# Kernel tuning notes

Measured on AMD Instinct MI355X. Metric: run time of the kernel, lower is better.

Reference implementation:

```python
import jax, jax.numpy as jnp
import numpy as np

B, S, D = 4, 2048, 512
H, DK = 8, 64
EPS = 1e-8


def setup_inputs() -> dict:
    key = jax.random.key(0)
    ks = jax.random.split(key, 11)
    sc = 1.0 / np.sqrt(D)
    Q = jax.random.normal(ks[0], (B, S, D), dtype=jnp.float32)
    # binary keep-mask over key positions, [B, S]
    attention_masks = (jax.random.uniform(ks[1], (B, S)) > 0.1).astype(jnp.float32)
    Wq = jax.random.normal(ks[2], (D, H * DK), dtype=jnp.float32) * sc
    bq = jax.random.normal(ks[3], (H * DK,), dtype=jnp.float32) * 0.01
    Wk = jax.random.normal(ks[4], (D, H * DK), dtype=jnp.float32) * sc
    bk = jax.random.normal(ks[5], (H * DK,), dtype=jnp.float32) * 0.01
    Wv = jax.random.normal(ks[6], (D, H * DK), dtype=jnp.float32) * sc
    bv = jax.random.normal(ks[7], (H * DK,), dtype=jnp.float32) * 0.01
    Wo = jax.random.normal(ks[8], (H * DK, D), dtype=jnp.float32) * (1.0 / np.sqrt(H * DK))
    bo = jax.random.normal(ks[9], (D,), dtype=jnp.float32) * 0.01
    return {"Q": Q, "attention_masks": attention_masks, "Wq": Wq, "bq": bq,
            "Wk": Wk, "bk": bk, "Wv": Wv, "bv": bv, "Wo": Wo, "bo": bo}


def reference(Q, attention_masks, Wq, bq, Wk, bk, Wv, bv, Wo, bo):
    b, s, _ = Q.shape
    # projections -> [B, H, S, DK]
    q = (Q @ Wq + bq).reshape(b, s, H, DK).transpose(0, 2, 1, 3)
    k = (Q @ Wk + bk).reshape(b, s, H, DK).transpose(0, 2, 1, 3)
    v = (Q @ Wv + bv).reshape(b, s, H, DK).transpose(0, 2, 1, 3)
    # scores: exp(QK^T / sqrt(dk)) * mask, normalized by row-sum (no max subtraction, matching source)
    scores = jnp.exp(jnp.einsum('bhqd,bhkd->bhqk', q, k) / np.sqrt(DK))
    scores = scores * attention_masks[:, None, None, :]  # mask broadcast over query dim
    attn = scores / (jnp.sum(scores, axis=-1, keepdims=True) + EPS)
    ctx = jnp.einsum('bhqk,bhkd->bhqd', attn, v)
    ctx = ctx.transpose(0, 2, 1, 3).reshape(b, s, H * DK)
    return ctx @ Wo + bo
```

## Files before the change

### kernel.cpp

```cpp
#include <hip/hip_runtime.h>
#include <math.h>

constexpr int NB = 4, NS = 2048, ND = 512, NH = 8, NDK = 64;
constexpr int NM = NB * NS, NHD = NH * NDK;

typedef short short8v __attribute__((ext_vector_type(8)));
typedef float f32x16v __attribute__((ext_vector_type(16)));
typedef unsigned int uint4v __attribute__((ext_vector_type(4)));

__device__ __forceinline__ unsigned short f2bf(float f) {
    unsigned u = __float_as_uint(f);
    return (unsigned short)((u + 0x7fffu + ((u >> 16) & 1u)) >> 16);
}
__device__ __forceinline__ float bf2f(unsigned short h) {
    return __uint_as_float(((unsigned)h) << 16);
}

#define MFMA32(a, b, c) __builtin_amdgcn_mfma_f32_32x32x16_bf16(a, b, c, 0, 0, 0)

__global__ __launch_bounds__(256) void split_x(
    const float* __restrict__ X, unsigned short* __restrict__ xh,
    unsigned short* __restrict__ xl)
{
    const size_t base = ((size_t)blockIdx.x * 256 + threadIdx.x) * 16;
#pragma unroll
    for (int j = 0; j < 4; ++j) {
        float4 v = *(const float4*)&X[base + 4 * j];
        ushort4 h, l;
        h.x = f2bf(v.x); h.y = f2bf(v.y); h.z = f2bf(v.z); h.w = f2bf(v.w);
        l.x = f2bf(v.x - bf2f(h.x)); l.y = f2bf(v.y - bf2f(h.y));
        l.z = f2bf(v.z - bf2f(h.z)); l.w = f2bf(v.w - bf2f(h.w));
        *(ushort4*)&xh[base + 4 * j] = h;
        *(ushort4*)&xl[base + 4 * j] = l;
    }
}

__global__ __launch_bounds__(256) void split_wT(
    const float* __restrict__ W0, const float* __restrict__ W1,
    const float* __restrict__ W2, const float* __restrict__ W3,
    unsigned short* __restrict__ wth, unsigned short* __restrict__ wtl)
{
    const int z = blockIdx.z;
    const float* W = (z == 0) ? W0 : (z == 1) ? W1 : (z == 2) ? W2 : W3;
    unsigned short* th = wth + (size_t)z * ND * ND;
    unsigned short* tl = wtl + (size_t)z * ND * ND;

    __shared__ float T[64][68];
    const int t = threadIdx.x;
    const int k0 = blockIdx.y * 64, n0 = blockIdx.x * 64;
    {
        const int r = t >> 2, c4 = (t & 3) * 16;
#pragma unroll
        for (int j = 0; j < 4; ++j)
            *(float4*)&T[r][c4 + 4 * j] = *(const float4*)&W[(size_t)(k0 + r) * ND + n0 + c4 + 4 * j];
    }
    __syncthreads();
    {
        const int r = t >> 2, c4 = (t & 3) * 16;
        unsigned short* dh = th + (size_t)(n0 + r) * ND + k0 + c4;
        unsigned short* dl = tl + (size_t)(n0 + r) * ND + k0 + c4;
#pragma unroll
        for (int j = 0; j < 4; ++j) {
            ushort4 h, l;
#pragma unroll
            for (int e = 0; e < 4; ++e) {
                float v = T[c4 + 4 * j + e][r];
                unsigned short hh = f2bf(v);
                ((unsigned short*)&h)[e] = hh;
                ((unsigned short*)&l)[e] = f2bf(v - bf2f(hh));
            }
            *(ushort4*)(dh + 4 * j) = h;
            *(ushort4*)(dl + 4 * j) = l;
        }
    }
}

__global__ __launch_bounds__(256, 2) void proj_qkv_mfma(
    const unsigned short* __restrict__ xh, const unsigned short* __restrict__ xl,
    const unsigned short* __restrict__ wth, const unsigned short* __restrict__ wtl,
    const float* __restrict__ bq, const float* __restrict__ bk,
    const float* __restrict__ bv,
    unsigned short* __restrict__ qh, unsigned short* __restrict__ ql,
    unsigned short* __restrict__ kh, unsigned short* __restrict__ kl,
    unsigned short* __restrict__ vh)
{
    constexpr int AH = 0, AL = 16384, BH = 32768, BL = 49152;
    __shared__ __align__(16) unsigned char smem[65536];

    const int z = blockIdx.z;
    const float* bias = (z == 0) ? bq : (z == 1) ? bk : bv;
    unsigned short* hp = (z == 0) ? qh : (z == 1) ? kh : vh;
    unsigned short* lp = (z == 0) ? ql : (z == 1) ? kl : (unsigned short*)0;
    const float sc = (z == 0) ? 0.18033688011112042f : 1.0f;
    const unsigned char* bth = (const unsigned char*)(wth + (size_t)z * ND * ND);
    const unsigned char* btl = (const unsigned char*)(wtl + (size_t)z * ND * ND);

    const int tid = threadIdx.x, lane = tid & 63, w = tid >> 6;
    const int wm = w >> 1, wn = w & 1;
    const int c = lane & 31, hi = lane >> 5;
    const int m0 = blockIdx.y * 128, n0 = blockIdx.x * 128;

    const unsigned char* ah_base = (const unsigned char*)xh;
    const unsigned char* al_base = (const unsigned char*)xl;

    int rr[4], gg[4], dd[4];
#pragma unroll
    for (int i = 0; i < 4; ++i) {
        int G = tid + 256 * i;
        rr[i] = G >> 3; gg[i] = G & 7;
        dd[i] = rr[i] * 128 + ((gg[i] ^ (rr[i] & 7)) * 16);
    }

    uint4v sah[4], sal[4], sbh[4], sbl[4];
    auto loads = [&](int kt) {
        const int kb = kt * 128;
#pragma unroll
        for (int i = 0; i < 4; ++i) {
            const size_t arow = (size_t)(m0 + rr[i]) * 1024 + kb + gg[i] * 16;
            const size_t brow = (size_t)(n0 + rr[i]) * 1024 + kb + gg[i] * 16;
            sah[i] = *(const uint4v*)(ah_base + arow);
            sal[i] = *(const uint4v*)(al_base + arow);
            sbh[i] = *(const uint4v*)(bth + brow);
            sbl[i] = *(const uint4v*)(btl + brow);
        }
    };
    auto writes = [&]() {
#pragma unroll
        for (int i = 0; i < 4; ++i) {
            *(uint4v*)(smem + AH + dd[i]) = sah[i];
            *(uint4v*)(smem + AL + dd[i]) = sal[i];
            *(uint4v*)(smem + BH + dd[i]) = sbh[i];
            *(uint4v*)(smem + BL + dd[i]) = sbl[i];
        }
    };

    f32x16v acc[2][2];
#pragma unroll
    for (int a = 0; a < 2; ++a)
#pragma unroll
        for (int bq2 = 0; bq2 < 2; ++bq2)
#pragma unroll
            for (int r = 0; r < 16; ++r) acc[a][bq2][r] = 0.f;

    loads(0);
    for (int kt = 0; kt < ND / 64; ++kt) {
        __syncthreads();
        writes();
        if (kt + 1 < ND / 64) loads(kt + 1);
        __syncthreads();
#pragma unroll
        for (int ks = 0; ks < 4; ++ks) {
            short8v afh[2], afl[2], bfh[2], bfl[2];
#pragma unroll
            for (int ms = 0; ms < 2; ++ms) {
                const int row = wm * 64 + ms * 32 + c;
                const int gb = row * 128 + (((2 * ks + hi) ^ (c & 7)) * 16);
                afh[ms] = *(const short8v*)(smem + AH + gb);
                afl[ms] = *(const short8v*)(smem + AL + gb);
            }
#pragma unroll
            for (int ns = 0; ns < 2; ++ns) {
                const int row = wn * 64 + ns * 32 + c;
                const int gb = row * 128 + (((2 * ks + hi) ^ (c & 7)) * 16);
                bfh[ns] = *(const short8v*)(smem + BH + gb);
                bfl[ns] = *(const short8v*)(smem + BL + gb);
            }
#pragma unroll
            for (int ms = 0; ms < 2; ++ms)
#pragma unroll
                for (int ns = 0; ns < 2; ++ns) {
                    acc[ms][ns] = MFMA32(afh[ms], bfh[ns], acc[ms][ns]);
                    acc[ms][ns] = MFMA32(afh[ms], bfl[ns], acc[ms][ns]);
                    acc[ms][ns] = MFMA32(afl[ms], bfh[ns], acc[ms][ns]);
                }
        }
    }

    const int b = m0 >> 11;
    const int s_base = (m0 & (NS - 1)) + wm * 64;
#pragma unroll
    for (int ns = 0; ns < 2; ++ns) {
        const int n = n0 + wn * 64 + ns * 32 + c;
        const int h = n >> 6, dk = n & (NDK - 1);
        const float bv4 = bias[n];
        const size_t bhBase = (size_t)(b * NH + h) * NS * NDK + dk;
#pragma unroll
        for (int ms = 0; ms < 2; ++ms)
#pragma unroll
            for (int r = 0; r < 16; ++r) {
                const int s = s_base + ms * 32 + (r & 3) + 8 * (r >> 2) + 4 * hi;
                const float v = (acc[ms][ns][r] + bv4) * sc;
                const unsigned short h0 = f2bf(v);
                hp[bhBase + (size_t)s * NDK] = h0;
                if (lp) lp[bhBase + (size_t)s * NDK] = f2bf(v - bf2f(h0));
            }
    }
}

__global__ __launch_bounds__(256) void vt_convert(
    const unsigned short* __restrict__ vh, unsigned short* __restrict__ vth)
{
    const int bh = blockIdx.y;
    const int s0 = blockIdx.x * 64;
    __shared__ unsigned short th[64][72];
    const int t = threadIdx.x;
    {
        const int sl = t & 63, ch = (t >> 6) * 16;
        const unsigned short* sh = vh + ((size_t)bh * NS + s0 + sl) * NDK + ch;
#pragma unroll
        for (int j = 0; j < 4; ++j)
            *(ushort4*)&th[sl][ch + 4 * j] = *(const ushort4*)(sh + 4 * j);
    }
    __syncthreads();
    {
        const int dv = t >> 2, sc = (t & 3) * 16;
        unsigned short* dh = vth + ((size_t)bh * NDK + dv) * NS + s0 + sc;
#pragma unroll
        for (int j = 0; j < 4; ++j) {
            ushort4 oh;
            oh.x = th[sc + 4 * j + 0][dv]; oh.y = th[sc + 4 * j + 1][dv];
            oh.z = th[sc + 4 * j + 2][dv]; oh.w = th[sc + 4 * j + 3][dv];
            *(ushort4*)(dh + 4 * j) = oh;
        }
    }
}

__global__ __launch_bounds__(256, 2) void attn(
    const unsigned short* __restrict__ qhp, const unsigned short* __restrict__ qlp,
    const unsigned short* __restrict__ khp, const unsigned short* __restrict__ klp,
    const unsigned short* __restrict__ vthp,
    const float* __restrict__ maskp,
    unsigned short* __restrict__ cth)
{
    constexpr int NT = NS / 64;
    constexpr int KH = 0, KL = 8192, VH = 16384, TILE = 24576;
    constexpr int P_OFF = 49152;
    __shared__ __align__(16) unsigned char smem[59392];

    const int tid = threadIdx.x, lane = tid & 63, w = tid >> 6;
    const int bid = blockIdx.x;
    const int xcd = bid & 7, r0 = bid >> 3;
    const int qt = r0 & 15, bh = xcd + 8 * (r0 >> 4);
    const int b = bh >> 3;
    const int q0 = qt * 128;
    const int c = lane & 31, hi = lane >> 5;
    const int csw = (c & 7) * 16;

    unsigned* Ph = (unsigned*)(smem + P_OFF + w * 2560);

    const unsigned char* kh_base = (const unsigned char*)khp + (size_t)bh * NS * 128;
    const unsigned char* kl_base = (const unsigned char*)klp + (size_t)bh * NS * 128;
    const unsigned char* vh_base = (const unsigned char*)vthp + (size_t)bh * 64 * 4096;

    const int G1 = tid, G2 = tid + 256;
    const int r1 = G1 >> 3, g1 = G1 & 7, r2 = G2 >> 3, g2 = G2 & 7;
    const int d1 = r1 * 128 + ((g1 ^ (r1 & 7)) * 16);
    const int d2 = r2 * 128 + ((g2 ^ (r2 & 7)) * 16);

    uint4v skh1, skl1, svh1, skh2, skl2, svh2;
    auto loads = [&](int kt) {
        const size_t ko = (size_t)kt * 8192;
        const size_t vo = (size_t)kt * 128;
        skh1 = *(const uint4v*)(kh_base + ko + (size_t)G1 * 16);
        skh2 = *(const uint4v*)(kh_base + ko + (size_t)G2 * 16);
        skl1 = *(const uint4v*)(kl_base + ko + (size_t)G1 * 16);
        skl2 = *(const uint4v*)(kl_base + ko + (size_t)G2 * 16);
        svh1 = *(const uint4v*)(vh_base + vo + (size_t)r1 * 4096 + g1 * 16);
        svh2 = *(const uint4v*)(vh_base + vo + (size_t)r2 * 4096 + g2 * 16);
    };
    auto writes = [&](unsigned char* buf) {
        *(uint4v*)(buf + KH + d1) = skh1;
        *(uint4v*)(buf + KH + d2) = skh2;
        *(uint4v*)(buf + KL + d1) = skl1;
        *(uint4v*)(buf + KL + d2) = skl2;
        *(uint4v*)(buf + VH + d1) = svh1;
        *(uint4v*)(buf + VH + d2) = svh2;
    };

    short8v qfh[4], qfl[4];
    {
        const unsigned short* qr  = qhp + ((size_t)bh * NS + q0 + 32 * w + c) * NDK + 8 * hi;
        const unsigned short* qrl = qlp + ((size_t)bh * NS + q0 + 32 * w + c) * NDK + 8 * hi;
#pragma unroll
        for (int km = 0; km < 4; ++km) {
            qfh[km] = *(const short8v*)(qr + km * 16);
            qfl[km] = *(const short8v*)(qrl + km * 16);
        }
    }

    f32x16v acc[2];
#pragma unroll
    for (int d = 0; d < 2; ++d)
#pragma unroll
        for (int r = 0; r < 16; ++r) acc[d][r] = 0.f;
    float dsp0 = 0.f, dsp1 = 0.f, dsp2 = 0.f, dsp3 = 0.f;

    auto compute = [&](const unsigned char* buf, int kt) {
#pragma unroll
        for (int kb = 0; kb < 2; ++kb) {
            short8v kfh[4], kfl[4];
            const int rowb = (32 * kb + c) * 128;
#pragma unroll
            for (int km = 0; km < 4; ++km) {
                const int gb = ((2 * km + hi) * 16) ^ csw;
                kfh[km] = *(const short8v*)(buf + KH + rowb + gb);
                kfl[km] = *(const short8v*)(buf + KL + rowb + gb);
            }
            f32x16v s0, s1;
#pragma unroll
            for (int r = 0; r < 16; ++r) { s0[r] = 0.f; s1[r] = 0.f; }
#pragma unroll
            for (int km = 0; km < 4; ++km) {
                s0 = MFMA32(kfh[km], qfh[km], s0);
                s1 = MFMA32(kfh[km], qfl[km], s1);
            }
#pragma unroll
            for (int km = 0; km < 4; ++km)
                s0 = MFMA32(kfl[km], qfh[km], s0);

            float pm[16];
#pragma unroll
            for (int rr2 = 0; rr2 < 4; ++rr2) {
                float4 mv = *(const float4*)&maskp[(size_t)b * NS + kt * 64 + 32 * kb + 8 * rr2 + 4 * hi];
                pm[4 * rr2 + 0] = mv.x; pm[4 * rr2 + 1] = mv.y;
                pm[4 * rr2 + 2] = mv.z; pm[4 * rr2 + 3] = mv.w;
            }
            unsigned wph[8];
#pragma unroll
            for (int p2 = 0; p2 < 8; ++p2) {
                float x0 = s0[2 * p2] + s1[2 * p2];
                float x1 = s0[2 * p2 + 1] + s1[2 * p2 + 1];
                float e0, e1;
                asm("v_exp_f32 %0, %1" : "=v"(e0) : "v"(x0));
                asm("v_exp_f32 %0, %1" : "=v"(e1) : "v"(x1));
                e0 *= pm[2 * p2];
                e1 *= pm[2 * p2 + 1];
                unsigned wv;
                asm("v_cvt_pk_bf16_f32 %0, %1, %2" : "=v"(wv) : "v"(e0), "v"(e1));
                wph[p2] = wv;
                float dlo = __uint_as_float(wv << 16);
                float dhi = __uint_as_float(wv & 0xffff0000u);
                if ((p2 & 3) == 0) dsp0 += dlo + dhi;
                else if ((p2 & 3) == 1) dsp1 += dlo + dhi;
                else if ((p2 & 3) == 2) dsp2 += dlo + dhi;
                else dsp3 += dlo + dhi;
            }
#pragma unroll
            for (int rr2 = 0; rr2 < 4; ++rr2) {
                uint2 th2; th2.x = wph[2 * rr2]; th2.y = wph[2 * rr2 + 1];
                *(uint2*)&Ph[c * 20 + 4 * rr2 + 2 * hi] = th2;
            }
            asm volatile("s_waitcnt lgkmcnt(0)" ::: "memory");
            __builtin_amdgcn_sched_barrier(0);
#pragma unroll
            for (int pc2 = 0; pc2 < 2; ++pc2) {
                const int pc = 2 * kb + pc2;
                uint4v th4 = *(const uint4v*)&Ph[c * 20 + 8 * pc2 + 4 * hi];
                short8v pfh = __builtin_bit_cast(short8v, th4);
                const int vgb = ((2 * pc + hi) * 16) ^ csw;
#pragma unroll
                for (int d = 0; d < 2; ++d) {
                    const int vrow = (32 * d + c) * 128;
                    short8v vfh = *(const short8v*)(buf + VH + vrow + vgb);
                    acc[d] = MFMA32(vfh, pfh, acc[d]);
                }
            }
        }
    };

    unsigned char* buf0 = smem;
    unsigned char* buf1 = smem + TILE;

    loads(0);
    writes(buf0);
    loads(1);
    __syncthreads();

    auto step = [&](int kt, unsigned char* rbuf, unsigned char* wbuf) {
        if (kt + 1 < NT) writes(wbuf);
        if (kt + 2 < NT) loads(kt + 2);
        compute(rbuf, kt);
        __syncthreads();
    };
    for (int kt = 0; kt < NT; kt += 2) {
        step(kt, buf0, buf1);
        step(kt + 1, buf1, buf0);
    }

    float dsum = (dsp0 + dsp1) + (dsp2 + dsp3);
    dsum += __shfl_xor(dsum, 32);
    const float inv = 1.0f / (dsum + 1e-8f);
    unsigned short* ohr = cth + (size_t)bh * 64 * NS + q0 + 32 * w + c;
#pragma unroll
    for (int d = 0; d < 2; ++d)
#pragma unroll
        for (int r = 0; r < 16; ++r) {
            const int dv = 32 * d + (r & 3) + 8 * (r >> 2) + 4 * hi;
            ohr[(size_t)dv * NS] = f2bf(acc[d][r] * inv);
        }
}

__global__ __launch_bounds__(256) void ctx_split(
    const unsigned short* __restrict__ cth, unsigned short* __restrict__ cnh)
{
    const int bh = blockIdx.y;
    const int b = bh >> 3, h = bh & 7;
    const int s0 = blockIdx.x * 64;
    __shared__ unsigned short th[64][72];
    const int t = threadIdx.x;
    {
        const int rd = t >> 2, sc = (t & 3) * 16;
        const unsigned short* sh = cth + ((size_t)bh * NDK + rd) * NS + s0 + sc;
#pragma unroll
        for (int j = 0; j < 4; ++j)
            *(ushort4*)&th[rd][sc + 4 * j] = *(const ushort4*)(sh + 4 * j);
    }
    __syncthreads();
    {
        const int sl = t >> 2, kc = (t & 3) * 16;
        const size_t m = (size_t)b * NS + s0 + sl;
        unsigned short* dh = cnh + m * NHD + h * NDK + kc;
#pragma unroll
        for (int j = 0; j < 4; ++j) {
            ushort4 hh;
#pragma unroll
            for (int e = 0; e < 4; ++e)
                ((unsigned short*)&hh)[e] = th[kc + 4 * j + e][sl];
            *(ushort4*)(dh + 4 * j) = hh;
        }
    }
}

__global__ __launch_bounds__(256, 2) void proj_out_mfma(
    const unsigned short* __restrict__ cnh,
    const unsigned short* __restrict__ wth, const unsigned short* __restrict__ wtl,
    const float* __restrict__ bo, float* __restrict__ out)
{
    constexpr int AH = 0, BH = 16384, BL = 32768;
    __shared__ __align__(16) unsigned char smem[49152];

    const int tid = threadIdx.x, lane = tid & 63, w = tid >> 6;
    const int wm = w >> 1, wn = w & 1;
    const int c = lane & 31, hi = lane >> 5;
    const int m0 = blockIdx.y * 128, n0 = blockIdx.x * 128;

    const unsigned char* ah_base = (const unsigned char*)cnh;
    const unsigned char* bth = (const unsigned char*)wth;
    const unsigned char* btl = (const unsigned char*)wtl;

    int rr[4], gg[4], dd[4];
#pragma unroll
    for (int i = 0; i < 4; ++i) {
        int G = tid + 256 * i;
        rr[i] = G >> 3; gg[i] = G & 7;
        dd[i] = rr[i] * 128 + ((gg[i] ^ (rr[i] & 7)) * 16);
    }

    uint4v sah[4], sbh[4], sbl[4];
    auto loads = [&](int kt) {
        const int kb = kt * 128;
#pragma unroll
        for (int i = 0; i < 4; ++i) {
            const size_t arow = (size_t)(m0 + rr[i]) * 1024 + kb + gg[i] * 16;
            const size_t brow = (size_t)(n0 + rr[i]) * 1024 + kb + gg[i] * 16;
            sah[i] = *(const uint4v*)(ah_base + arow);
            sbh[i] = *(const uint4v*)(bth + brow);
            sbl[i] = *(const uint4v*)(btl + brow);
        }
    };
    auto writes = [&]() {
#pragma unroll
        for (int i = 0; i < 4; ++i) {
            *(uint4v*)(smem + AH + dd[i]) = sah[i];
            *(uint4v*)(smem + BH + dd[i]) = sbh[i];
            *(uint4v*)(smem + BL + dd[i]) = sbl[i];
        }
    };

    f32x16v acc[2][2];
#pragma unroll
    for (int a = 0; a < 2; ++a)
#pragma unroll
        for (int bq2 = 0; bq2 < 2; ++bq2)
#pragma unroll
            for (int r = 0; r < 16; ++r) acc[a][bq2][r] = 0.f;

    loads(0);
    for (int kt = 0; kt < NHD / 64; ++kt) {
        __syncthreads();
        writes();
        if (kt + 1 < NHD / 64) loads(kt + 1);
        __syncthreads();
#pragma unroll
        for (int ks = 0; ks < 4; ++ks) {
            short8v afh[2], bfh[2], bfl[2];
#pragma unroll
            for (int ms = 0; ms < 2; ++ms) {
                const int row = wm * 64 + ms * 32 + c;
                const int gb = row * 128 + (((2 * ks + hi) ^ (c & 7)) * 16);
                afh[ms] = *(const short8v*)(smem + AH + gb);
            }
#pragma unroll
            for (int ns = 0; ns < 2; ++ns) {
                const int row = wn * 64 + ns * 32 + c;
                const int gb = row * 128 + (((2 * ks + hi) ^ (c & 7)) * 16);
                bfh[ns] = *(const short8v*)(smem + BH + gb);
                bfl[ns] = *(const short8v*)(smem + BL + gb);
            }
#pragma unroll
            for (int ms = 0; ms < 2; ++ms)
#pragma unroll
                for (int ns = 0; ns < 2; ++ns) {
                    acc[ms][ns] = MFMA32(afh[ms], bfh[ns], acc[ms][ns]);
                    acc[ms][ns] = MFMA32(afh[ms], bfl[ns], acc[ms][ns]);
                }
        }
    }

#pragma unroll
    for (int ns = 0; ns < 2; ++ns) {
        const int n = n0 + wn * 64 + ns * 32 + c;
        const float bv4 = bo[n];
#pragma unroll
        for (int ms = 0; ms < 2; ++ms)
#pragma unroll
            for (int r = 0; r < 16; ++r) {
                const int m = m0 + wm * 64 + ms * 32 + (r & 3) + 8 * (r >> 2) + 4 * hi;
                out[(size_t)m * ND + n] = acc[ms][ns][r] + bv4;
            }
    }
}

extern "C" void kernel_launch(void* const* d_in, const int* in_sizes, int n_in,
                              void* d_out, int out_size, void* d_ws, size_t ws_size,
                              hipStream_t stream) {
    const float* Q    = (const float*)d_in[0];
    const float* mask = (const float*)d_in[1];
    const float* Wq   = (const float*)d_in[2];
    const float* bq   = (const float*)d_in[3];
    const float* Wk   = (const float*)d_in[4];
    const float* bk   = (const float*)d_in[5];
    const float* Wv   = (const float*)d_in[6];
    const float* bv   = (const float*)d_in[7];
    const float* Wo   = (const float*)d_in[8];
    const float* bo   = (const float*)d_in[9];

    unsigned char* W = (unsigned char*)d_ws;
    constexpr size_t MB = 1048576;
    unsigned short* xh   = (unsigned short*)(W + 0);
    unsigned short* xl   = (unsigned short*)(W + 8 * MB);
    unsigned short* wtH  = (unsigned short*)(W + 16 * MB);
    unsigned short* wtL  = (unsigned short*)(W + 18 * MB);
    unsigned short* qh   = (unsigned short*)(W + 20 * MB);
    unsigned short* ql   = (unsigned short*)(W + 28 * MB);
    unsigned short* kh   = (unsigned short*)(W + 36 * MB);
    unsigned short* kl   = (unsigned short*)(W + 44 * MB);
    unsigned short* vh   = (unsigned short*)(W + 52 * MB);
    unsigned short* vth  = (unsigned short*)(W + 0);
    unsigned short* cth  = (unsigned short*)(W + 8 * MB);
    unsigned short* cnh  = (unsigned short*)(W + 20 * MB);

    split_x<<<NM * ND / (256 * 16), 256, 0, stream>>>(Q, xh, xl);
    split_wT<<<dim3(8, 8, 4), 256, 0, stream>>>(Wq, Wk, Wv, Wo, wtH, wtL);

    proj_qkv_mfma<<<dim3(NHD / 128, NM / 128, 3), 256, 0, stream>>>(
        xh, xl, wtH, wtL, bq, bk, bv, qh, ql, kh, kl, vh);

    vt_convert<<<dim3(NS / 64, NB * NH), 256, 0, stream>>>(vh, vth);

    attn<<<512, 256, 0, stream>>>(qh, ql, kh, kl, vth, mask, cth);

    ctx_split<<<dim3(NS / 64, NB * NH), 256, 0, stream>>>(cth, cnh);

    proj_out_mfma<<<dim3(ND / 128, NM / 128), 256, 0, stream>>>(
        cnh, wtH + (size_t)3 * ND * ND, wtL + (size_t)3 * ND * ND,
        bo, (float*)d_out);
}
```

Baseline: 238.9 us.

## Single-buffer attention LDS tiles to raise occupancy to four blocks per CU

Replaces the double-buffered K/V shared-memory tiles in the attention kernel with a single buffer, shrinking LDS from about 58KB to 34KB, and raises launch bounds to four blocks per CU. The loop now computes on the buffer, synchronizes, writes the prefetched registers, issues the next global loads, and synchronizes again. The aim is to hide latency through more resident waves rather than intra-block double buffering. In exchange each tile iteration needs two barriers and can no longer overlap its LDS writes with compute, and the tighter register budget may cause spills.

```diff
diff --git a/kernel.cpp b/kernel.cpp
--- a/kernel.cpp
+++ b/kernel.cpp
@@ -225,7 +225,7 @@
     }
 }
 
-__global__ __launch_bounds__(256, 2) void attn(
+__global__ __launch_bounds__(256, 4) void attn(
     const unsigned short* __restrict__ qhp, const unsigned short* __restrict__ qlp,
     const unsigned short* __restrict__ khp, const unsigned short* __restrict__ klp,
     const unsigned short* __restrict__ vthp,
@@ -233,9 +233,9 @@
     unsigned short* __restrict__ cth)
 {
     constexpr int NT = NS / 64;
-    constexpr int KH = 0, KL = 8192, VH = 16384, TILE = 24576;
-    constexpr int P_OFF = 49152;
-    __shared__ __align__(16) unsigned char smem[59392];
+    constexpr int KH = 0, KL = 8192, VH = 16384;
+    constexpr int P_OFF = 24576;
+    __shared__ __align__(16) unsigned char smem[34816];
 
     const int tid = threadIdx.x, lane = tid & 63, w = tid >> 6;
     const int bid = blockIdx.x;
@@ -268,13 +268,13 @@
         svh1 = *(const uint4v*)(vh_base + vo + (size_t)r1 * 4096 + g1 * 16);
         svh2 = *(const uint4v*)(vh_base + vo + (size_t)r2 * 4096 + g2 * 16);
     };
-    auto writes = [&](unsigned char* buf) {
-        *(uint4v*)(buf + KH + d1) = skh1;
-        *(uint4v*)(buf + KH + d2) = skh2;
-        *(uint4v*)(buf + KL + d1) = skl1;
-        *(uint4v*)(buf + KL + d2) = skl2;
-        *(uint4v*)(buf + VH + d1) = svh1;
-        *(uint4v*)(buf + VH + d2) = svh2;
+    auto writes = [&]() {
+        *(uint4v*)(smem + KH + d1) = skh1;
+        *(uint4v*)(smem + KH + d2) = skh2;
+        *(uint4v*)(smem + KL + d1) = skl1;
+        *(uint4v*)(smem + KL + d2) = skl2;
+        *(uint4v*)(smem + VH + d1) = svh1;
+        *(uint4v*)(smem + VH + d2) = svh2;
     };
 
     short8v qfh[4], qfl[4];
@@ -295,7 +295,7 @@
         for (int r = 0; r < 16; ++r) acc[d][r] = 0.f;
     float dsp0 = 0.f, dsp1 = 0.f, dsp2 = 0.f, dsp3 = 0.f;
 
-    auto compute = [&](const unsigned char* buf, int kt) {
+    auto compute = [&](int kt) {
 #pragma unroll
         for (int kb = 0; kb < 2; ++kb) {
             short8v kfh[4], kfl[4];
@@ -303,8 +303,8 @@
 #pragma unroll
             for (int km = 0; km < 4; ++km) {
                 const int gb = ((2 * km + hi) * 16) ^ csw;
-                kfh[km] = *(const short8v*)(buf + KH + rowb + gb);
-                kfl[km] = *(const short8v*)(buf + KL + rowb + gb);
+                kfh[km] = *(const short8v*)(smem + KH + rowb + gb);
+                kfl[km] = *(const short8v*)(smem + KL + rowb + gb);
             }
             f32x16v s0, s1;
 #pragma unroll
@@ -361,30 +361,26 @@
 #pragma unroll
                 for (int d = 0; d < 2; ++d) {
                     const int vrow = (32 * d + c) * 128;
-                    short8v vfh = *(const short8v*)(buf + VH + vrow + vgb);
+                    short8v vfh = *(const short8v*)(smem + VH + vrow + vgb);
                     acc[d] = MFMA32(vfh, pfh, acc[d]);
                 }
             }
         }
     };
 
-    unsigned char* buf0 = smem;
-    unsigned char* buf1 = smem + TILE;
-
     loads(0);
-    writes(buf0);
+    writes();
     loads(1);
     __syncthreads();
 
-    auto step = [&](int kt, unsigned char* rbuf, unsigned char* wbuf) {
-        if (kt + 1 < NT) writes(wbuf);
-        if (kt + 2 < NT) loads(kt + 2);
-        compute(rbuf, kt);
-        __syncthreads();
-    };
-    for (int kt = 0; kt < NT; kt += 2) {
-        step(kt, buf0, buf1);
-        step(kt + 1, buf1, buf0);
+    for (int kt = 0; kt < NT; ++kt) {
+        compute(kt);
+        if (kt + 1 < NT) {
+            __syncthreads();
+            writes();
+            if (kt + 2 < NT) loads(kt + 2);
+            __syncthreads();
+        }
     }
 
     float dsum = (dsp0 + dsp1) + (dsp2 + dsp3);
```

Measured after the change: 399.7 us. 67.3% more time.
